# Optimization experiments

Hardware: AMD Instinct MI355X
Metric: run time of the kernel (lower is better)

## Reference

```python
import jax, jax.numpy as jnp
import numpy as np

B, S, D, H, FF = 1, 2048, 2048, 32, 8192
HD = D // H
SCALING = HD ** -0.5
WBITS, ABITS = 8, 8
NEG = jnp.finfo(jnp.float32).min


def ste_round(x):
    # straight-through estimator round
    return x + jax.lax.stop_gradient(jnp.round(x) - x)


def fake_quant(x, bits, axis):
    # min-max asymmetric fake quantization (OmniQuant-style dynamic quant)
    qmax = float(2 ** bits - 1)
    xmin = jnp.minimum(jnp.min(x, axis=axis, keepdims=True), 0.0)
    xmax = jnp.maximum(jnp.max(x, axis=axis, keepdims=True), 0.0)
    scale = jnp.maximum((xmax - xmin) / qmax, 1e-5)
    zp = jnp.round(-xmin / scale)
    q = jnp.clip(ste_round(x / scale) + zp, 0.0, qmax)
    return (q - zp) * scale


def qlinear(x, W, b):
    # QuantLinear: quantize activation per-token, weight per-output-channel
    xq = fake_quant(x, ABITS, -1)
    Wq = fake_quant(W, WBITS, 1)  # W: [out, in], per-row (output channel)
    return xq @ Wq.T + b


def layernorm(x, g, b):
    mu = jnp.mean(x, axis=-1, keepdims=True)
    var = jnp.var(x, axis=-1, keepdims=True)
    return (x - mu) * jax.lax.rsqrt(var + 1e-5) * g + b


def setup_inputs():
    key = jax.random.key(0)
    ks = jax.random.split(key, 16)
    w = lambda k, shape: (jax.random.normal(k, shape) * 0.02).astype(jnp.float32)
    hidden_states = jax.random.normal(ks[0], (B, S, D), dtype=jnp.float32)
    causal = jnp.tril(jnp.ones((S, S), dtype=bool))
    attention_mask = jnp.where(causal, 0.0, NEG)[None, None].astype(jnp.float32)
    attention_mask = jnp.broadcast_to(attention_mask, (B, 1, S, S))
    return {
        'hidden_states': hidden_states,
        'attention_mask': attention_mask,
        'Wq': w(ks[1], (D, D)), 'bq': jnp.zeros((D,), jnp.float32),
        'Wk': w(ks[2], (D, D)), 'bk': jnp.zeros((D,), jnp.float32),
        'Wv': w(ks[3], (D, D)), 'bv': jnp.zeros((D,), jnp.float32),
        'Wo': w(ks[4], (D, D)), 'bo': jnp.zeros((D,), jnp.float32),
        'ln1_g': jnp.ones((D,), jnp.float32), 'ln1_b': jnp.zeros((D,), jnp.float32),
        'W1': w(ks[5], (FF, D)), 'b1': jnp.zeros((FF,), jnp.float32),
        'W2': w(ks[6], (D, FF)), 'b2': jnp.zeros((D,), jnp.float32),
        'ln2_g': jnp.ones((D,), jnp.float32), 'ln2_b': jnp.zeros((D,), jnp.float32),
    }


def _split_heads(x):
    # [B,S,D] -> [B,H,S,HD]
    return x.reshape(B, S, H, HD).transpose(0, 2, 1, 3)


def _layer(hidden_states, attention_mask, Wq, bq, Wk, bk, Wv, bv, Wo, bo,
           ln1_g, ln1_b, W1, b1, W2, b2, ln2_g, ln2_b):
    # ---- self attention block (do_layer_norm_before=True) ----
    residual = hidden_states
    x = layernorm(hidden_states, ln1_g, ln1_b)

    q = qlinear(x, Wq, bq) * SCALING
    q = fake_quant(q, ABITS, -1)          # qkt_matmul.quant_x1
    k = qlinear(x, Wk, bk)
    k = fake_quant(k, ABITS, -1)          # qkt_matmul.quant_x2
    v = qlinear(x, Wv, bv)
    v = fake_quant(v, ABITS, -1)          # pv_matmul.quant_x2

    qh, kh, vh = _split_heads(q), _split_heads(k), _split_heads(v)
    scores = jnp.einsum('bhqd,bhkd->bhqk', qh, kh)  # [B,H,S,S]
    scores = scores + attention_mask
    scores = jnp.maximum(scores, NEG)
    probs = jax.nn.softmax(scores, axis=-1)
    probs = fake_quant(probs, ABITS, -1)  # pv_matmul.quant_x1
    ctx = jnp.einsum('bhqk,bhkd->bhqd', probs, vh)
    ctx = ctx.transpose(0, 2, 1, 3).reshape(B, S, D)
    attn_out = qlinear(ctx, Wo, bo)
    hidden_states = residual + attn_out

    # ---- FFN block ----
    residual = hidden_states
    x = layernorm(hidden_states, ln2_g, ln2_b)
    x = jax.nn.relu(qlinear(x, W1, b1))
    x = qlinear(x, W2, b2)
    return residual + x


def reference(hidden_states, attention_mask, Wq, bq, Wk, bk, Wv, bv, Wo, bo,
              ln1_g, ln1_b, W1, b1, W2, b2, ln2_g, ln2_b):
    return _layer(hidden_states, attention_mask, Wq, bq, Wk, bk, Wv, bv, Wo, bo,
                  ln1_g, ln1_b, W1, b1, W2, b2, ln2_g, ln2_b)
```

## Files before the change

kernel.cpp:

```cpp
#include <hip/hip_runtime.h>
#include <hip/hip_bf16.h>
#include <math.h>

#define S_LEN 2048
#define D_DIM 2048
#define H_NUM 32
#define HD_DIM 64
#define FF_DIM 8192
#define QMAX 255.0f
#define LOG2E 1.4426950408889634f

typedef __attribute__((ext_vector_type(4))) float f32x4;
typedef __attribute__((ext_vector_type(4))) int i32x4;
typedef __attribute__((ext_vector_type(8))) __bf16 bf16x8;
typedef unsigned short u16;
typedef signed char i8;

__device__ __forceinline__ u16 f32i_to_bf16(float v) {
  return (u16)(__float_as_uint(v) >> 16);
}
__device__ __forceinline__ u16 f32_to_bf16_rne(float v) {
  __bf16 b = (__bf16)v;
  return *(u16*)&b;
}
__device__ __forceinline__ float bf16_to_f32(u16 u) {
  return __uint_as_float((unsigned int)u << 16);
}
__device__ __forceinline__ int pack4_i8(float q0, float q1, float q2, float q3) {
  int c0 = (int)q0 - 128, c1 = (int)q1 - 128, c2 = (int)q2 - 128, c3 = (int)q3 - 128;
  return (c0 & 0xFF) | ((c1 & 0xFF) << 8) | ((c2 & 0xFF) << 16) | ((c3 & 0xFF) << 24);
}

__device__ __forceinline__ float wred_sum(float v) {
#pragma unroll
  for (int o = 1; o < 64; o <<= 1) v += __shfl_xor(v, o, 64);
  return v;
}
__device__ __forceinline__ float wred_min(float v) {
#pragma unroll
  for (int o = 1; o < 64; o <<= 1) v = fminf(v, __shfl_xor(v, o, 64));
  return v;
}
__device__ __forceinline__ float wred_max(float v) {
#pragma unroll
  for (int o = 1; o < 64; o <<= 1) v = fmaxf(v, __shfl_xor(v, o, 64));
  return v;
}

__device__ __forceinline__ void gload_lds16(const void* g, void* l) {
  __builtin_amdgcn_global_load_lds(
      (__attribute__((address_space(1))) void*)(g),
      (__attribute__((address_space(3))) void*)(l), 16, 0, 0);
}

__device__ __forceinline__ void xcd_swz(int& bx, int& by) {
  const int gx = gridDim.x;
  const int nwg = gx * gridDim.y;
  const int orig = blockIdx.x + gx * blockIdx.y;
  const int swz = (orig & 7) * (nwg >> 3) + (orig >> 3);
  bx = swz % gx;
  by = swz / gx;
}

__global__ __launch_bounds__(256) void ln_quant_i8(const float* __restrict__ x,
                                                   const float* __restrict__ g,
                                                   const float* __restrict__ bvec,
                                                   i8* __restrict__ out,
                                                   float* __restrict__ srow,
                                                   float* __restrict__ zrow,
                                                   float* __restrict__ S0row,
                                                   float* __restrict__ S1row) {
  __shared__ float red[8];
  const int row = blockIdx.x, tid = threadIdx.x;
  const float4* xr = (const float4*)(x + (size_t)row * D_DIM);
  const float4* g4 = (const float4*)g;
  const float4* b4 = (const float4*)bvec;

  float4 v0 = xr[tid], v1 = xr[tid + 256];
  float s = v0.x + v0.y + v0.z + v0.w + v1.x + v1.y + v1.z + v1.w;
  float ss = v0.x * v0.x + v0.y * v0.y + v0.z * v0.z + v0.w * v0.w +
             v1.x * v1.x + v1.y * v1.y + v1.z * v1.z + v1.w * v1.w;
  s = wred_sum(s); ss = wred_sum(ss);
  if ((tid & 63) == 0) { red[tid >> 6] = s; red[4 + (tid >> 6)] = ss; }
  __syncthreads();
  float mu = (red[0] + red[1] + red[2] + red[3]) / (float)D_DIM;
  float var = (red[4] + red[5] + red[6] + red[7]) / (float)D_DIM - mu * mu;
  float rstd = 1.0f / sqrtf(var + 1e-5f);
  __syncthreads();

  float mn = 0.f, mx = 0.f;
  float4 n0, n1;
  {
    float4 gg = g4[tid], bb = b4[tid];
    n0.x = (v0.x - mu) * rstd * gg.x + bb.x; n0.y = (v0.y - mu) * rstd * gg.y + bb.y;
    n0.z = (v0.z - mu) * rstd * gg.z + bb.z; n0.w = (v0.w - mu) * rstd * gg.w + bb.w;
    gg = g4[tid + 256]; bb = b4[tid + 256];
    n1.x = (v1.x - mu) * rstd * gg.x + bb.x; n1.y = (v1.y - mu) * rstd * gg.y + bb.y;
    n1.z = (v1.z - mu) * rstd * gg.z + bb.z; n1.w = (v1.w - mu) * rstd * gg.w + bb.w;
    mn = fminf(mn, fminf(fminf(n0.x, n0.y), fminf(n0.z, n0.w)));
    mn = fminf(mn, fminf(fminf(n1.x, n1.y), fminf(n1.z, n1.w)));
    mx = fmaxf(mx, fmaxf(fmaxf(n0.x, n0.y), fmaxf(n0.z, n0.w)));
    mx = fmaxf(mx, fmaxf(fmaxf(n1.x, n1.y), fmaxf(n1.z, n1.w)));
  }
  mn = wred_min(mn); mx = wred_max(mx);
  if ((tid & 63) == 0) { red[tid >> 6] = mn; red[4 + (tid >> 6)] = mx; }
  __syncthreads();
  mn = fminf(fminf(red[0], red[1]), fminf(red[2], red[3]));
  mx = fmaxf(fmaxf(red[4], red[5]), fmaxf(red[6], red[7]));
  float scale = fmaxf((mx - mn) / QMAX, 1e-5f);
  float zp = rintf(-mn / scale);
  if (tid == 0) { srow[row] = scale; zrow[row] = 128.0f - zp; }

  float q00 = fminf(fmaxf(rintf(n0.x / scale) + zp, 0.f), QMAX);
  float q01 = fminf(fmaxf(rintf(n0.y / scale) + zp, 0.f), QMAX);
  float q02 = fminf(fmaxf(rintf(n0.z / scale) + zp, 0.f), QMAX);
  float q03 = fminf(fmaxf(rintf(n0.w / scale) + zp, 0.f), QMAX);
  float q10 = fminf(fmaxf(rintf(n1.x / scale) + zp, 0.f), QMAX);
  float q11 = fminf(fmaxf(rintf(n1.y / scale) + zp, 0.f), QMAX);
  float q12 = fminf(fmaxf(rintf(n1.z / scale) + zp, 0.f), QMAX);
  float q13 = fminf(fmaxf(rintf(n1.w / scale) + zp, 0.f), QMAX);
  *(int*)&out[(size_t)row * D_DIM + tid * 4] = pack4_i8(q00, q01, q02, q03);
  *(int*)&out[(size_t)row * D_DIM + 1024 + tid * 4] = pack4_i8(q10, q11, q12, q13);
  float s0 = q00 + q01 + q02 + q03 - 512.f;
  float s1 = q10 + q11 + q12 + q13 - 512.f;
  __syncthreads();
  s0 = wred_sum(s0); s1 = wred_sum(s1);
  if ((tid & 63) == 0) { red[tid >> 6] = s0; red[4 + (tid >> 6)] = s1; }
  __syncthreads();
  if (tid == 0) {
    S0row[row] = red[0] + red[1] + red[2] + red[3];
    S1row[row] = red[4] + red[5] + red[6] + red[7];
  }
}

__global__ __launch_bounds__(256) void act_quant_i8(const float* __restrict__ x,
                                                    i8* __restrict__ out,
                                                    float* __restrict__ srow,
                                                    float* __restrict__ zrow,
                                                    float* __restrict__ S0row,
                                                    float* __restrict__ S1row) {
  __shared__ float red[8];
  const int row = blockIdx.x, tid = threadIdx.x;
  const float4* xr = (const float4*)(x + (size_t)row * D_DIM);
  float4 n0 = xr[tid], n1 = xr[tid + 256];
  float mn = 0.f, mx = 0.f;
  mn = fminf(mn, fminf(fminf(n0.x, n0.y), fminf(n0.z, n0.w)));
  mn = fminf(mn, fminf(fminf(n1.x, n1.y), fminf(n1.z, n1.w)));
  mx = fmaxf(mx, fmaxf(fmaxf(n0.x, n0.y), fmaxf(n0.z, n0.w)));
  mx = fmaxf(mx, fmaxf(fmaxf(n1.x, n1.y), fmaxf(n1.z, n1.w)));
  mn = wred_min(mn); mx = wred_max(mx);
  if ((tid & 63) == 0) { red[tid >> 6] = mn; red[4 + (tid >> 6)] = mx; }
  __syncthreads();
  mn = fminf(fminf(red[0], red[1]), fminf(red[2], red[3]));
  mx = fmaxf(fmaxf(red[4], red[5]), fmaxf(red[6], red[7]));
  float scale = fmaxf((mx - mn) / QMAX, 1e-5f);
  float zp = rintf(-mn / scale);
  if (tid == 0) { srow[row] = scale; zrow[row] = 128.0f - zp; }
  float q00 = fminf(fmaxf(rintf(n0.x / scale) + zp, 0.f), QMAX);
  float q01 = fminf(fmaxf(rintf(n0.y / scale) + zp, 0.f), QMAX);
  float q02 = fminf(fmaxf(rintf(n0.z / scale) + zp, 0.f), QMAX);
  float q03 = fminf(fmaxf(rintf(n0.w / scale) + zp, 0.f), QMAX);
  float q10 = fminf(fmaxf(rintf(n1.x / scale) + zp, 0.f), QMAX);
  float q11 = fminf(fmaxf(rintf(n1.y / scale) + zp, 0.f), QMAX);
  float q12 = fminf(fmaxf(rintf(n1.z / scale) + zp, 0.f), QMAX);
  float q13 = fminf(fmaxf(rintf(n1.w / scale) + zp, 0.f), QMAX);
  *(int*)&out[(size_t)row * D_DIM + tid * 4] = pack4_i8(q00, q01, q02, q03);
  *(int*)&out[(size_t)row * D_DIM + 1024 + tid * 4] = pack4_i8(q10, q11, q12, q13);
  float s0 = q00 + q01 + q02 + q03 - 512.f;
  float s1 = q10 + q11 + q12 + q13 - 512.f;
  __syncthreads();
  s0 = wred_sum(s0); s1 = wred_sum(s1);
  if ((tid & 63) == 0) { red[tid >> 6] = s0; red[4 + (tid >> 6)] = s1; }
  __syncthreads();
  if (tid == 0) {
    S0row[row] = red[0] + red[1] + red[2] + red[3];
    S1row[row] = red[4] + red[5] + red[6] + red[7];
  }
}

__device__ __forceinline__ void wquant_body(const float* __restrict__ wr0,
                                            i8* __restrict__ wo,
                                            float* __restrict__ sc,
                                            float* __restrict__ zc,
                                            float* __restrict__ S0c,
                                            float* __restrict__ S1c,
                                            int row, int K) {
  __shared__ float red[8];
  const int tid = threadIdx.x;
  const float4* wr = (const float4*)wr0;
  const int K4 = K >> 2, H4 = K4 >> 1;
  float mn = 0.f, mx = 0.f;
  for (int i = tid; i < K4; i += 256) {
    float4 v = wr[i];
    mn = fminf(mn, fminf(fminf(v.x, v.y), fminf(v.z, v.w)));
    mx = fmaxf(mx, fmaxf(fmaxf(v.x, v.y), fmaxf(v.z, v.w)));
  }
  mn = wred_min(mn); mx = wred_max(mx);
  if ((tid & 63) == 0) { red[tid >> 6] = mn; red[4 + (tid >> 6)] = mx; }
  __syncthreads();
  mn = fminf(fminf(red[0], red[1]), fminf(red[2], red[3]));
  mx = fmaxf(fmaxf(red[4], red[5]), fmaxf(red[6], red[7]));
  float scale = fmaxf((mx - mn) / QMAX, 1e-5f);
  float zp = rintf(-mn / scale);
  if (tid == 0) { sc[row] = scale; zc[row] = 128.0f - zp; }
  float s0 = 0.f, s1 = 0.f;
  for (int i = tid; i < K4; i += 256) {
    float4 v = wr[i];
    float q0 = fminf(fmaxf(rintf(v.x / scale) + zp, 0.f), QMAX);
    float q1 = fminf(fmaxf(rintf(v.y / scale) + zp, 0.f), QMAX);
    float q2 = fminf(fmaxf(rintf(v.z / scale) + zp, 0.f), QMAX);
    float q3 = fminf(fmaxf(rintf(v.w / scale) + zp, 0.f), QMAX);
    *(int*)&wo[i * 4] = pack4_i8(q0, q1, q2, q3);
    float gs = q0 + q1 + q2 + q3 - 512.f;
    if (i < H4) s0 += gs; else s1 += gs;
  }
  __syncthreads();
  s0 = wred_sum(s0); s1 = wred_sum(s1);
  if ((tid & 63) == 0) { red[tid >> 6] = s0; red[4 + (tid >> 6)] = s1; }
  __syncthreads();
  if (tid == 0) {
    S0c[row] = red[0] + red[1] + red[2] + red[3];
    S1c[row] = red[4] + red[5] + red[6] + red[7];
  }
}

__global__ __launch_bounds__(256) void wquant_i8(const float* __restrict__ W,
                                                 i8* __restrict__ Wi,
                                                 float* __restrict__ sc,
                                                 float* __restrict__ zc,
                                                 float* __restrict__ S0c,
                                                 float* __restrict__ S1c, int K) {
  const int row = blockIdx.x;
  wquant_body(W + (size_t)row * K, Wi + (size_t)row * K, sc, zc, S0c, S1c, row, K);
}

__global__ __launch_bounds__(256) void wquant4_i8(
    const float* __restrict__ W0, i8* __restrict__ O0, float* s0, float* z0, float* a0, float* b0,
    const float* __restrict__ W1, i8* __restrict__ O1, float* s1, float* z1, float* a1, float* b1,
    const float* __restrict__ W2, i8* __restrict__ O2, float* s2, float* z2, float* a2, float* b2,
    const float* __restrict__ W3, i8* __restrict__ O3, float* s3, float* z3, float* a3, float* b3) {
  const int which = blockIdx.x >> 11;
  const int row = blockIdx.x & (D_DIM - 1);
  const float* W = (which == 0) ? W0 : (which == 1) ? W1 : (which == 2) ? W2 : W3;
  i8* O = (which == 0) ? O0 : (which == 1) ? O1 : (which == 2) ? O2 : O3;
  float* sc = (which == 0) ? s0 : (which == 1) ? s1 : (which == 2) ? s2 : s3;
  float* zc = (which == 0) ? z0 : (which == 1) ? z1 : (which == 2) ? z2 : z3;
  float* Sa = (which == 0) ? a0 : (which == 1) ? a1 : (which == 2) ? a2 : a3;
  float* Sb = (which == 0) ? b0 : (which == 1) ? b1 : (which == 2) ? b2 : b3;
  wquant_body(W + (size_t)row * D_DIM, O + (size_t)row * D_DIM, sc, zc, Sa, Sb, row, D_DIM);
}

__global__ __launch_bounds__(256) void requant3(
    const u16* __restrict__ qv, const float* __restrict__ tqmn, const float* __restrict__ tqmx,
    u16* __restrict__ qo, float* __restrict__ sqv,
    const u16* __restrict__ kv, const float* __restrict__ tkmn, const float* __restrict__ tkmx,
    u16* __restrict__ ko, float* __restrict__ skv,
    const u16* __restrict__ vv, const float* __restrict__ tvmn, const float* __restrict__ tvmx,
    u16* __restrict__ vo) {
  __shared__ float red[8];
  const int wh = blockIdx.x >> 11;
  const int row = blockIdx.x & (S_LEN - 1);
  const int tid = threadIdx.x;
  const u16* vals = (wh == 0) ? qv : (wh == 1) ? kv : vv;
  const float* tmn = (wh == 0) ? tqmn : (wh == 1) ? tkmn : tvmn;
  const float* tmx = (wh == 0) ? tqmx : (wh == 1) ? tkmx : tvmx;
  u16* out = (wh == 0) ? qo : (wh == 1) ? ko : vo;
  float* srow = (wh == 0) ? sqv : (wh == 1) ? skv : nullptr;
  const int value_mode = (wh == 2) ? 1 : 0;

  float mn = 0.f, mx = 0.f;
  if (tid < 32) {
    mn = tmn[(size_t)row * 32 + tid];
    mx = tmx[(size_t)row * 32 + tid];
  }
  mn = wred_min(mn); mx = wred_max(mx);
  if ((tid & 63) == 0) { red[tid >> 6] = mn; red[4 + (tid >> 6)] = mx; }
  __syncthreads();
  mn = fminf(fminf(red[0], red[1]), fminf(red[2], red[3]));
  mx = fmaxf(fmaxf(red[4], red[5]), fmaxf(red[6], red[7]));
  mn = fminf(mn, 0.f); mx = fmaxf(mx, 0.f);
  float scale = fmaxf((mx - mn) / QMAX, 1e-5f);
  float zp = rintf(-mn / scale);
  if (srow && tid == 0) srow[row] = scale;
  const ushort4* vr = (const ushort4*)(vals + (size_t)row * D_DIM);
  ushort4* orow = (ushort4*)(out + (size_t)row * D_DIM);
  for (int i = tid; i < D_DIM / 4; i += 256) {
    ushort4 u = vr[i];
    float q0 = fminf(fmaxf(rintf(bf16_to_f32(u.x) / scale) + zp, 0.f), QMAX) - zp;
    float q1 = fminf(fmaxf(rintf(bf16_to_f32(u.y) / scale) + zp, 0.f), QMAX) - zp;
    float q2 = fminf(fmaxf(rintf(bf16_to_f32(u.z) / scale) + zp, 0.f), QMAX) - zp;
    float q3 = fminf(fmaxf(rintf(bf16_to_f32(u.w) / scale) + zp, 0.f), QMAX) - zp;
    ushort4 o;
    if (value_mode) {
      o.x = f32_to_bf16_rne(q0 * scale); o.y = f32_to_bf16_rne(q1 * scale);
      o.z = f32_to_bf16_rne(q2 * scale); o.w = f32_to_bf16_rne(q3 * scale);
    } else {
      o.x = f32i_to_bf16(q0); o.y = f32i_to_bf16(q1);
      o.z = f32i_to_bf16(q2); o.w = f32i_to_bf16(q3);
    }
    orow[i] = o;
  }
}

__global__ __launch_bounds__(256) void transpose_v(const u16* __restrict__ vfb,
                                                   u16* __restrict__ vtb) {
  __shared__ u16 Ts[64][66];
  const int j0 = blockIdx.x * 64;
  const int h = blockIdx.y;
  const int tid = threadIdx.x;
  for (int c = tid; c < 512; c += 256) {
    int r = c >> 3, ch = c & 7;
    *(float4*)&Ts[r][ch * 8] =
        *(const float4*)&vfb[(size_t)(j0 + r) * D_DIM + h * HD_DIM + ch * 8];
  }
  __syncthreads();
  for (int c = tid; c < 512; c += 256) {
    int d = c >> 3, ch = c & 7;
    u16 tmp[8];
#pragma unroll
    for (int e = 0; e < 8; ++e) tmp[e] = Ts[ch * 8 + e][d];
    *(float4*)&vtb[(size_t)(h * HD_DIM + d) * S_LEN + j0 + ch * 8] = *(float4*)tmp;
  }
}

__global__ __launch_bounds__(256) void requant_ff_i8(const u16* __restrict__ vals,
                                                     const float* __restrict__ tmx,
                                                     i8* __restrict__ out,
                                                     float* __restrict__ srow,
                                                     float* __restrict__ zrow,
                                                     float* __restrict__ S0row,
                                                     float* __restrict__ S1row) {
  __shared__ float red[8];
  const int row = blockIdx.x, tid = threadIdx.x;
  float mx = (tid < 128) ? tmx[(size_t)row * 128 + tid] : 0.f;
  mx = wred_max(mx);
  if ((tid & 63) == 0) red[tid >> 6] = mx;
  __syncthreads();
  mx = fmaxf(fmaxf(red[0], red[1]), fmaxf(red[2], red[3]));
  mx = fmaxf(mx, 0.f);
  float scale = fmaxf(mx / QMAX, 1e-5f);
  if (tid == 0) { srow[row] = scale; zrow[row] = 128.0f; }
  const ushort4* vr = (const ushort4*)(vals + (size_t)row * FF_DIM);
  const int N4 = FF_DIM >> 2;
  float s0 = 0.f, s1 = 0.f;
  for (int i = tid; i < N4; i += 256) {
    ushort4 u = vr[i];
    float q0 = fminf(fmaxf(rintf(bf16_to_f32(u.x) / scale), 0.f), QMAX);
    float q1 = fminf(fmaxf(rintf(bf16_to_f32(u.y) / scale), 0.f), QMAX);
    float q2 = fminf(fmaxf(rintf(bf16_to_f32(u.z) / scale), 0.f), QMAX);
    float q3 = fminf(fmaxf(rintf(bf16_to_f32(u.w) / scale), 0.f), QMAX);
    *(int*)&out[(size_t)row * FF_DIM + i * 4] = pack4_i8(q0, q1, q2, q3);
    float gs = q0 + q1 + q2 + q3 - 512.f;
    if (i < 1024) s0 += gs; else s1 += gs;
  }
  __syncthreads();
  s0 = wred_sum(s0); s1 = wred_sum(s1);
  if ((tid & 63) == 0) { red[tid >> 6] = s0; red[4 + (tid >> 6)] = s1; }
  __syncthreads();
  if (tid == 0) {
    S0row[row] = red[0] + red[1] + red[2] + red[3];
    S1row[row] = red[4] + red[5] + red[6] + red[7];
  }
}

__device__ __forceinline__ void gemm128_i8_db(
    const i8* __restrict__ A, const i8* __restrict__ B,
    int K, int bm, int bn, int k_begin, int k_end,
    i8* As, i8* Bs, i32x4 (&acc)[4][4]) {
  const int tid = threadIdx.x;
  const int wid = tid >> 6, lane = tid & 63;
  const int wr = wid >> 1, wc = wid & 1;
  const int lr = lane & 15, lk = lane >> 4;
  const int r0 = tid >> 2, c0 = (tid & 3) * 16;
  const int r1 = 64 + r0;
  const size_t ldsb0 = (size_t)(wid * 64) * 16;
  const size_t ldsb1 = (size_t)(256 + wid * 64) * 16;

  const i8* Ag0 = A + (size_t)(bm + r0) * K + c0;
  const i8* Ag1 = A + (size_t)(bm + r1) * K + c0;
  const i8* Bg0 = B + (size_t)(bn + r0) * K + c0;
  const i8* Bg1 = B + (size_t)(bn + r1) * K + c0;

  const int nt = (k_end - k_begin) >> 6;

#define STAGE_I8(t)                                   \
  {                                                   \
    const int _k = k_begin + (t) * 64;                \
    i8* _Ab = As + (size_t)((t) & 1) * 8192;          \
    i8* _Bb = Bs + (size_t)((t) & 1) * 8192;          \
    gload_lds16(Ag0 + _k, _Ab + ldsb0);               \
    gload_lds16(Ag1 + _k, _Ab + ldsb1);               \
    gload_lds16(Bg0 + _k, _Bb + ldsb0);               \
    gload_lds16(Bg1 + _k, _Bb + ldsb1);               \
  }

  STAGE_I8(0);
  __syncthreads();

  for (int t = 0; t < nt; ++t) {
    const i8* Ac = As + (size_t)(t & 1) * 8192;
    const i8* Bc = Bs + (size_t)(t & 1) * 8192;
    i32x4 af[4], bf[4];
// ... 173 lines not shown
#pragma unroll
      for (int r = 0; r < 4; ++r)
        dst[(size_t)(rbase + mi * 16 + r) * D_DIM + col] = (float)acc[mi][ni][r];
  }
}

__global__ __launch_bounds__(256) void splitk_reduce4(
    const float* __restrict__ part,
    const float* __restrict__ sxa, const float* __restrict__ zxa,
    const float* __restrict__ Sxa0, const float* __restrict__ Sxa1,
    const float* __restrict__ sw, const float* __restrict__ zw,
    const float* __restrict__ Sw0, const float* __restrict__ Sw1,
    float Kf, const float* __restrict__ bias, const float* __restrict__ res,
    float* __restrict__ out) {
  const size_t st4 = (size_t)S_LEN * D_DIM / 4;
  for (size_t i = (size_t)blockIdx.x * 256 + threadIdx.x; i < st4;
       i += (size_t)gridDim.x * 256) {
    const int row = (int)(i >> 9);
    const int c4 = (int)(i & 511);
    float4 s = ((const float4*)part)[i];
    float4 p1 = ((const float4*)part)[i + st4];
    float4 p2 = ((const float4*)part)[i + 2 * st4];
    float4 p3 = ((const float4*)part)[i + 3 * st4];
    s.x += p1.x + p2.x + p3.x; s.y += p1.y + p2.y + p3.y;
    s.z += p1.z + p2.z + p3.z; s.w += p1.w + p2.w + p3.w;
    const float sxr = sxa[row], zxr = zxa[row];
    const float Sxr = Sxa0[row] + Sxa1[row];
    float4 ws = ((const float4*)sw)[c4];
    float4 wz = ((const float4*)zw)[c4];
    float4 w0 = ((const float4*)Sw0)[c4];
    float4 w1 = ((const float4*)Sw1)[c4];
    float4 b4 = ((const float4*)bias)[c4];
    float4 o;
    o.x = sxr * ws.x * (s.x + zxr * (w0.x + w1.x) + wz.x * Sxr + Kf * zxr * wz.x) + b4.x;
    o.y = sxr * ws.y * (s.y + zxr * (w0.y + w1.y) + wz.y * Sxr + Kf * zxr * wz.y) + b4.y;
    o.z = sxr * ws.z * (s.z + zxr * (w0.z + w1.z) + wz.z * Sxr + Kf * zxr * wz.z) + b4.z;
    o.w = sxr * ws.w * (s.w + zxr * (w0.w + w1.w) + wz.w * Sxr + Kf * zxr * wz.w) + b4.w;
    if (res) {
      float4 r = ((const float4*)res)[i];
      o.x += r.x; o.y += r.y; o.z += r.z; o.w += r.w;
    }
    ((float4*)out)[i] = o;
  }
}

__global__ __launch_bounds__(256) void splitk_reduce_ln(
    const float* __restrict__ part,
    const float* __restrict__ sxa, const float* __restrict__ zxa,
    const float* __restrict__ Sxa0, const float* __restrict__ Sxa1,
    const float* __restrict__ sw, const float* __restrict__ zw,
    const float* __restrict__ Sw0, const float* __restrict__ Sw1,
    const float* __restrict__ bias, const float* __restrict__ res,
    float* __restrict__ h2out,
    const float* __restrict__ g, const float* __restrict__ bvec,
    i8* __restrict__ out, float* __restrict__ srow, float* __restrict__ zrow,
    float* __restrict__ S0row, float* __restrict__ S1row) {
  __shared__ float red[8];
  const int row = blockIdx.x, tid = threadIdx.x;
  const size_t st = (size_t)S_LEN * D_DIM;
  const float4* p0 = (const float4*)(part + (size_t)row * D_DIM);
  const float4* p1 = (const float4*)(part + st + (size_t)row * D_DIM);
  const float4* p2 = (const float4*)(part + 2 * st + (size_t)row * D_DIM);
  const float4* p3 = (const float4*)(part + 3 * st + (size_t)row * D_DIM);
  const float4* rr = (const float4*)(res + (size_t)row * D_DIM);
  const float4* b4 = (const float4*)bias;
  const float4* g4 = (const float4*)g;
  const float4* e4 = (const float4*)bvec;

  const float sxr = sxa[row], zxr = zxa[row];
  const float Sxr = Sxa0[row] + Sxa1[row];

  float4 v0, v1;
#pragma unroll
  for (int h = 0; h < 2; ++h) {
    const int idx = tid + h * 256;
    float4 a = p0[idx], q = p1[idx], u = p2[idx], w = p3[idx];
    float4 ws = ((const float4*)sw)[idx];
    float4 wz = ((const float4*)zw)[idx];
    float4 s0 = ((const float4*)Sw0)[idx];
    float4 s1 = ((const float4*)Sw1)[idx];
    float4 bb = b4[idx], rv = rr[idx];
    float4 o;
    o.x = sxr * ws.x * (a.x + q.x + u.x + w.x + zxr * (s0.x + s1.x) + wz.x * Sxr + 2048.0f * zxr * wz.x) + bb.x + rv.x;
    o.y = sxr * ws.y * (a.y + q.y + u.y + w.y + zxr * (s0.y + s1.y) + wz.y * Sxr + 2048.0f * zxr * wz.y) + bb.y + rv.y;
    o.z = sxr * ws.z * (a.z + q.z + u.z + w.z + zxr * (s0.z + s1.z) + wz.z * Sxr + 2048.0f * zxr * wz.z) + bb.z + rv.z;
    o.w = sxr * ws.w * (a.w + q.w + u.w + w.w + zxr * (s0.w + s1.w) + wz.w * Sxr + 2048.0f * zxr * wz.w) + bb.w + rv.w;
    if (h == 0) v0 = o; else v1 = o;
  }
  float* h2r = h2out + (size_t)row * D_DIM;
  *(float4*)&h2r[tid * 4] = v0;
  *(float4*)&h2r[1024 + tid * 4] = v1;

  float s = v0.x + v0.y + v0.z + v0.w + v1.x + v1.y + v1.z + v1.w;
  float ss = v0.x * v0.x + v0.y * v0.y + v0.z * v0.z + v0.w * v0.w +
             v1.x * v1.x + v1.y * v1.y + v1.z * v1.z + v1.w * v1.w;
  s = wred_sum(s); ss = wred_sum(ss);
  if ((tid & 63) == 0) { red[tid >> 6] = s; red[4 + (tid >> 6)] = ss; }
  __syncthreads();
  float mu = (red[0] + red[1] + red[2] + red[3]) / (float)D_DIM;
  float var = (red[4] + red[5] + red[6] + red[7]) / (float)D_DIM - mu * mu;
  float rstd = 1.0f / sqrtf(var + 1e-5f);
  __syncthreads();

  float mn = 0.f, mx = 0.f;
  float4 n0, n1;
  {
    float4 gg = g4[tid], bb = e4[tid];
    n0.x = (v0.x - mu) * rstd * gg.x + bb.x; n0.y = (v0.y - mu) * rstd * gg.y + bb.y;
    n0.z = (v0.z - mu) * rstd * gg.z + bb.z; n0.w = (v0.w - mu) * rstd * gg.w + bb.w;
    gg = g4[tid + 256]; bb = e4[tid + 256];
    n1.x = (v1.x - mu) * rstd * gg.x + bb.x; n1.y = (v1.y - mu) * rstd * gg.y + bb.y;
    n1.z = (v1.z - mu) * rstd * gg.z + bb.z; n1.w = (v1.w - mu) * rstd * gg.w + bb.w;
    mn = fminf(mn, fminf(fminf(n0.x, n0.y), fminf(n0.z, n0.w)));
    mn = fminf(mn, fminf(fminf(n1.x, n1.y), fminf(n1.z, n1.w)));
    mx = fmaxf(mx, fmaxf(fmaxf(n0.x, n0.y), fmaxf(n0.z, n0.w)));
    mx = fmaxf(mx, fmaxf(fmaxf(n1.x, n1.y), fmaxf(n1.z, n1.w)));
  }
  mn = wred_min(mn); mx = wred_max(mx);
  if ((tid & 63) == 0) { red[tid >> 6] = mn; red[4 + (tid >> 6)] = mx; }
  __syncthreads();
  mn = fminf(fminf(red[0], red[1]), fminf(red[2], red[3]));
  mx = fmaxf(fmaxf(red[4], red[5]), fmaxf(red[6], red[7]));
  float scale = fmaxf((mx - mn) / QMAX, 1e-5f);
  float zp = rintf(-mn / scale);
  if (tid == 0) { srow[row] = scale; zrow[row] = 128.0f - zp; }
  float q00 = fminf(fmaxf(rintf(n0.x / scale) + zp, 0.f), QMAX);
  float q01 = fminf(fmaxf(rintf(n0.y / scale) + zp, 0.f), QMAX);
  float q02 = fminf(fmaxf(rintf(n0.z / scale) + zp, 0.f), QMAX);
  float q03 = fminf(fmaxf(rintf(n0.w / scale) + zp, 0.f), QMAX);
  float q10 = fminf(fmaxf(rintf(n1.x / scale) + zp, 0.f), QMAX);
  float q11 = fminf(fmaxf(rintf(n1.y / scale) + zp, 0.f), QMAX);
  float q12 = fminf(fmaxf(rintf(n1.z / scale) + zp, 0.f), QMAX);
  float q13 = fminf(fmaxf(rintf(n1.w / scale) + zp, 0.f), QMAX);
  *(int*)&out[(size_t)row * D_DIM + tid * 4] = pack4_i8(q00, q01, q02, q03);
  *(int*)&out[(size_t)row * D_DIM + 1024 + tid * 4] = pack4_i8(q10, q11, q12, q13);
  float s0 = q00 + q01 + q02 + q03 - 512.f;
  float s1 = q10 + q11 + q12 + q13 - 512.f;
  __syncthreads();
  s0 = wred_sum(s0); s1 = wred_sum(s1);
  if ((tid & 63) == 0) { red[tid >> 6] = s0; red[4 + (tid >> 6)] = s1; }
  __syncthreads();
  if (tid == 0) {
    S0row[row] = red[0] + red[1] + red[2] + red[3];
    S1row[row] = red[4] + red[5] + red[6] + red[7];
  }
}

__global__ __launch_bounds__(256) void attn_ml(
    const u16* __restrict__ qi, const float* __restrict__ sq,
    const u16* __restrict__ ki, const float* __restrict__ sk,
    float* __restrict__ Mb, float* __restrict__ Lb) {
  __shared__ __align__(16) u16 Ks[64][72];
  const int bid = blockIdx.x;
  const int ti = (S_LEN / 64 - 1) - (bid >> 5);
  const int h = bid & (H_NUM - 1);
  const int i0 = ti * 64;
  const int tid = threadIdx.x;
  const int wid = tid >> 6, lane = tid & 63;
  const int lr = lane & 15, g = lane >> 4;
  const size_t hbase = (size_t)h * HD_DIM;

  const int r_a = tid >> 3, ch_a = tid & 7;
  const int r_b = 32 + r_a;

  const bf16x8 aq0 = *(const bf16x8*)&qi[(size_t)(i0 + wid * 16 + lr) * D_DIM + hbase + g * 8];
  const bf16x8 aq1 = *(const bf16x8*)&qi[(size_t)(i0 + wid * 16 + lr) * D_DIM + hbase + 32 + g * 8];
  float sq2[4];
#pragma unroll
  for (int r = 0; r < 4; ++r) sq2[r] = sq[i0 + wid * 16 + g * 4 + r] * LOG2E;

  const int ntiles = i0 / 64 + 1;
  float m_r[4] = {-1e30f, -1e30f, -1e30f, -1e30f};
  float l_r[4] = {0.f, 0.f, 0.f, 0.f};

  float4 ka0 = *(const float4*)&ki[(size_t)r_a * D_DIM + hbase + ch_a * 8];
  float4 ka1 = *(const float4*)&ki[(size_t)r_b * D_DIM + hbase + ch_a * 8];
  for (int t = 0; t < ntiles; ++t) {
    __syncthreads();
    *(float4*)&Ks[r_a][ch_a * 8] = ka0;
    *(float4*)&Ks[r_b][ch_a * 8] = ka1;
    __syncthreads();
    if (t + 1 < ntiles) {
      const int jn = (t + 1) * 64;
      ka0 = *(const float4*)&ki[(size_t)(jn + r_a) * D_DIM + hbase + ch_a * 8];
      ka1 = *(const float4*)&ki[(size_t)(jn + r_b) * D_DIM + hbase + ch_a * 8];
    }

    f32x4 accs[4] = {};
#pragma unroll
    for (int ni = 0; ni < 4; ++ni) {
      bf16x8 b0 = *(const bf16x8*)&Ks[ni * 16 + lr][g * 8];
      bf16x8 b1 = *(const bf16x8*)&Ks[ni * 16 + lr][32 + g * 8];
      accs[ni] = __builtin_amdgcn_mfma_f32_16x16x32_bf16(aq0, b0, accs[ni], 0, 0, 0);
      accs[ni] = __builtin_amdgcn_mfma_f32_16x16x32_bf16(aq1, b1, accs[ni], 0, 0, 0);
    }

    const int jt = t * 64;
    float tv[4][4];
#pragma unroll
    for (int ni = 0; ni < 4; ++ni) {
      const float skc = sk[jt + ni * 16 + lr];
#pragma unroll
      for (int r = 0; r < 4; ++r) tv[ni][r] = accs[ni][r] * sq2[r] * skc;
    }
    if (t == ntiles - 1) {
      const int jcol = jt + lr, irow = i0 + wid * 16 + g * 4;
#pragma unroll
      for (int ni = 0; ni < 4; ++ni)
#pragma unroll
        for (int r = 0; r < 4; ++r)
          if (jcol + ni * 16 > irow + r) tv[ni][r] = -1e30f;
    }
#pragma unroll
    for (int r = 0; r < 4; ++r) {
      float tmax = fmaxf(fmaxf(tv[0][r], tv[1][r]), fmaxf(tv[2][r], tv[3][r]));
      tmax = fmaxf(tmax, __shfl_xor(tmax, 1, 64));
      tmax = fmaxf(tmax, __shfl_xor(tmax, 2, 64));
      tmax = fmaxf(tmax, __shfl_xor(tmax, 4, 64));
      tmax = fmaxf(tmax, __shfl_xor(tmax, 8, 64));
      float mnew = fmaxf(m_r[r], tmax);
      float sum = exp2f(tv[0][r] - mnew) + exp2f(tv[1][r] - mnew) +
                  exp2f(tv[2][r] - mnew) + exp2f(tv[3][r] - mnew);
      sum += __shfl_xor(sum, 1, 64);
      sum += __shfl_xor(sum, 2, 64);
      sum += __shfl_xor(sum, 4, 64);
      sum += __shfl_xor(sum, 8, 64);
      l_r[r] = l_r[r] * exp2f(m_r[r] - mnew) + sum;
      m_r[r] = mnew;
    }
  }

  if (lr == 0) {
#pragma unroll
    for (int r = 0; r < 4; ++r) {
      const int row = i0 + wid * 16 + g * 4 + r;
      Mb[(size_t)h * S_LEN + row] = m_r[r];
      Lb[(size_t)h * S_LEN + row] = l_r[r];
    }
  }
}

__global__ __launch_bounds__(256) void attn_pv(
    const u16* __restrict__ qi, const float* __restrict__ sq,
    const u16* __restrict__ ki, const float* __restrict__ sk,
    const u16* __restrict__ vt,
    const float* __restrict__ Mb, const float* __restrict__ Lb,
    float* __restrict__ ctx) {
  __shared__ __align__(16) u16 Ks[64][72];
  __shared__ __align__(16) u16 Ps[64][72];
  __shared__ __align__(16) u16 Vt[64][72];
  const int bid = blockIdx.x;
  const int ti = (S_LEN / 64 - 1) - (bid >> 5);
  const int h = bid & (H_NUM - 1);
  const int i0 = ti * 64;
  const int tid = threadIdx.x;
  const int wid = tid >> 6, lane = tid & 63;
  const int lr = lane & 15, g = lane >> 4;
  const size_t hbase = (size_t)h * HD_DIM;
  const size_t vtbase = (size_t)h * HD_DIM * S_LEN;

  const int r_a = tid >> 3, ch_a = tid & 7;
  const int r_b = 32 + r_a;

  const bf16x8 aq0 = *(const bf16x8*)&qi[(size_t)(i0 + wid * 16 + lr) * D_DIM + hbase + g * 8];
  const bf16x8 aq1 = *(const bf16x8*)&qi[(size_t)(i0 + wid * 16 + lr) * D_DIM + hbase + 32 + g * 8];

  float sq2[4], b_r[4], qsc[4];
#pragma unroll
  for (int r = 0; r < 4; ++r) {
    const int row = i0 + wid * 16 + g * 4 + r;
    sq2[r] = sq[row] * LOG2E;
    float m_t = Mb[(size_t)h * S_LEN + row];
    float li = Lb[(size_t)h * S_LEN + row];
    float sc = fmaxf((1.0f / li) / QMAX, 1e-5f);
    qsc[r] = sc;
    b_r[r] = m_t - log2f(1.0f / (li * sc));
  }

  const int ntiles = i0 / 64 + 1;
  f32x4 acco[4] = {};
  float4 kb0 = *(const float4*)&ki[(size_t)r_a * D_DIM + hbase + ch_a * 8];
  float4 kb1 = *(const float4*)&ki[(size_t)r_b * D_DIM + hbase + ch_a * 8];
  float4 vb0 = *(const float4*)&vt[vtbase + (size_t)r_a * S_LEN + ch_a * 8];
  float4 vb1 = *(const float4*)&vt[vtbase + (size_t)r_b * S_LEN + ch_a * 8];
  for (int t = 0; t < ntiles; ++t) {
    __syncthreads();
    *(float4*)&Ks[r_a][ch_a * 8] = kb0;
    *(float4*)&Ks[r_b][ch_a * 8] = kb1;
    *(float4*)&Vt[r_a][ch_a * 8] = vb0;
    *(float4*)&Vt[r_b][ch_a * 8] = vb1;
    __syncthreads();
    if (t + 1 < ntiles) {
      const int jn = (t + 1) * 64;
      kb0 = *(const float4*)&ki[(size_t)(jn + r_a) * D_DIM + hbase + ch_a * 8];
      kb1 = *(const float4*)&ki[(size_t)(jn + r_b) * D_DIM + hbase + ch_a * 8];
      vb0 = *(const float4*)&vt[vtbase + (size_t)r_a * S_LEN + jn + ch_a * 8];
      vb1 = *(const float4*)&vt[vtbase + (size_t)r_b * S_LEN + jn + ch_a * 8];
    }

    f32x4 accs[4] = {};
#pragma unroll
    for (int ni = 0; ni < 4; ++ni) {
      bf16x8 b0 = *(const bf16x8*)&Ks[ni * 16 + lr][g * 8];
      bf16x8 b1 = *(const bf16x8*)&Ks[ni * 16 + lr][32 + g * 8];
      accs[ni] = __builtin_amdgcn_mfma_f32_16x16x32_bf16(aq0, b0, accs[ni], 0, 0, 0);
      accs[ni] = __builtin_amdgcn_mfma_f32_16x16x32_bf16(aq1, b1, accs[ni], 0, 0, 0);
    }

    const int jt = t * 64;
    const bool diag = (t == ntiles - 1);
    const int jcol = jt + lr, irow = i0 + wid * 16 + g * 4;
#pragma unroll
    for (int ni = 0; ni < 4; ++ni) {
      const float skc = sk[jt + ni * 16 + lr];
#pragma unroll
      for (int r = 0; r < 4; ++r) {
        float tvv = accs[ni][r] * sq2[r] * skc;
        if (diag && (jcol + ni * 16 > irow + r)) tvv = -1e30f;
        float q8 = fminf(rintf(exp2f(tvv - b_r[r])), QMAX);
        Ps[wid * 16 + g * 4 + r][ni * 16 + lr] = f32i_to_bf16(q8);
      }
    }

    bf16x8 ap0 = *(const bf16x8*)&Ps[wid * 16 + lr][g * 8];
    bf16x8 ap1 = *(const bf16x8*)&Ps[wid * 16 + lr][32 + g * 8];
#pragma unroll
    for (int ni = 0; ni < 4; ++ni) {
      bf16x8 b0 = *(const bf16x8*)&Vt[ni * 16 + lr][g * 8];
      bf16x8 b1 = *(const bf16x8*)&Vt[ni * 16 + lr][32 + g * 8];
      acco[ni] = __builtin_amdgcn_mfma_f32_16x16x32_bf16(ap0, b0, acco[ni], 0, 0, 0);
      acco[ni] = __builtin_amdgcn_mfma_f32_16x16x32_bf16(ap1, b1, acco[ni], 0, 0, 0);
    }
  }

#pragma unroll
  for (int ni = 0; ni < 4; ++ni)
#pragma unroll
    for (int r = 0; r < 4; ++r) {
      const int row = i0 + wid * 16 + g * 4 + r;
      ctx[(size_t)row * D_DIM + hbase + ni * 16 + lr] = acco[ni][r] * qsc[r];
    }
}

extern "C" void kernel_launch(void* const* d_in, const int* in_sizes, int n_in,
                              void* d_out, int out_size, void* d_ws, size_t ws_size,
                              hipStream_t stream) {
  (void)in_sizes; (void)n_in; (void)out_size;
  const float* hs  = (const float*)d_in[0];
  const float* Wq  = (const float*)d_in[2];
  const float* bq  = (const float*)d_in[3];
  const float* Wk  = (const float*)d_in[4];
  const float* bk  = (const float*)d_in[5];
  const float* Wv  = (const float*)d_in[6];
  const float* bv  = (const float*)d_in[7];
  const float* Wo  = (const float*)d_in[8];
  const float* bo  = (const float*)d_in[9];
  const float* g1  = (const float*)d_in[10];
  const float* be1 = (const float*)d_in[11];
  const float* W1  = (const float*)d_in[12];
  const float* bf1 = (const float*)d_in[13];
  const float* W2  = (const float*)d_in[14];
  const float* bf2 = (const float*)d_in[15];
  const float* g2  = (const float*)d_in[16];
  const float* be2 = (const float*)d_in[17];
  float* out = (float*)d_out;

  const size_t SD = (size_t)S_LEN * D_DIM;
  const size_t SF = (size_t)S_LEN * FF_DIM;
  const size_t HS = (size_t)H_NUM * S_LEN;

  char* p = (char*)d_ws;
  auto alloc = [&](size_t bytes) { char* r = p; p += (bytes + 255) & ~(size_t)255; return r; };

  float* h2   = (float*)alloc(SD * 4);
  float* sx   = (float*)alloc(S_LEN * 4);
  float* zx   = (float*)alloc(S_LEN * 4);
  float* Sx0  = (float*)alloc(S_LEN * 4);
  float* Sx1  = (float*)alloc(S_LEN * 4);
  float* sy   = (float*)alloc(S_LEN * 4);
  float* zy   = (float*)alloc(S_LEN * 4);
  float* Sy0  = (float*)alloc(S_LEN * 4);
  float* Sy1  = (float*)alloc(S_LEN * 4);
  float* sxf  = (float*)alloc(S_LEN * 4);
  float* zxf  = (float*)alloc(S_LEN * 4);
  float* Sf0  = (float*)alloc(S_LEN * 4);
  float* Sf1  = (float*)alloc(S_LEN * 4);
  float* sqv  = (float*)alloc(S_LEN * 4);
  float* skv  = (float*)alloc(S_LEN * 4);
  float* Mb   = (float*)alloc(HS * 4);
  float* Lbv  = (float*)alloc(HS * 4);
  float* swq = (float*)alloc(D_DIM * 4); float* zwq = (float*)alloc(D_DIM * 4);
  float* Sq0 = (float*)alloc(D_DIM * 4); float* Sq1 = (float*)alloc(D_DIM * 4);
  float* swk = (float*)alloc(D_DIM * 4); float* zwk = (float*)alloc(D_DIM * 4);
  float* Sk0 = (float*)alloc(D_DIM * 4); float* Sk1 = (float*)alloc(D_DIM * 4);
  float* swv = (float*)alloc(D_DIM * 4); float* zwv = (float*)alloc(D_DIM * 4);
  float* Sv0 = (float*)alloc(D_DIM * 4); float* Sv1 = (float*)alloc(D_DIM * 4);
  float* swo = (float*)alloc(D_DIM * 4); float* zwo = (float*)alloc(D_DIM * 4);
  float* So0 = (float*)alloc(D_DIM * 4); float* So1 = (float*)alloc(D_DIM * 4);
  float* sw1 = (float*)alloc(FF_DIM * 4); float* zw1 = (float*)alloc(FF_DIM * 4);
  float* S10 = (float*)alloc(FF_DIM * 4); float* S11 = (float*)alloc(FF_DIM * 4);
  float* sw2 = (float*)alloc(D_DIM * 4); float* zw2 = (float*)alloc(D_DIM * 4);
  float* S20 = (float*)alloc(D_DIM * 4); float* S21 = (float*)alloc(D_DIM * 4);
  float* tqmn = (float*)alloc(S_LEN * 32 * 4);
  float* tqmx = (float*)alloc(S_LEN * 32 * 4);
  float* tkmn = (float*)alloc(S_LEN * 32 * 4);
  float* tkmx = (float*)alloc(S_LEN * 32 * 4);
  float* tvmn = (float*)alloc(S_LEN * 32 * 4);
  float* tvmx = (float*)alloc(S_LEN * 32 * 4);
  float* tf1x = (float*)alloc(S_LEN * 128 * 4);
  i8* xi  = (i8*)alloc(SD);
  i8* wqi = (i8*)alloc(SD);
  i8* wki = (i8*)alloc(SD);
  i8* wvi = (i8*)alloc(SD);
  i8* woi = (i8*)alloc(SD);
  i8* w1i = (i8*)alloc(SF);
  i8* w2i = (i8*)alloc(SF);
  i8* f1i = (i8*)alloc(SF);
  char* arena = alloc(8 * SD * 2);
  u16* qv   = (u16*)arena;
  u16* kv   = qv + SD;
  u16* vv   = kv + SD;
  u16* qi8  = vv + SD;
  u16* ki8  = qi8 + SD;
  u16* vfb  = ki8 + SD;
  float* ctxb = (float*)(vfb + SD);
  u16* vtb  = qv;
  float* pwo = (float*)arena;
  u16* f1v = (u16*)arena;
  float* pw2 = (float*)arena;
  size_t need = (size_t)(p - (char*)d_ws);
  if (ws_size < need) return;

  dim3 blk(256);

  wquant4_i8<<<4 * D_DIM, blk, 0, stream>>>(
      Wq, wqi, swq, zwq, Sq0, Sq1,
      Wk, wki, swk, zwk, Sk0, Sk1,
      Wv, wvi, swv, zwv, Sv0, Sv1,
      Wo, woi, swo, zwo, So0, So1);
  wquant_i8<<<FF_DIM, blk, 0, stream>>>(W1, w1i, sw1, zw1, S10, S11, D_DIM);
  wquant_i8<<<D_DIM, blk, 0, stream>>>(W2, w2i, sw2, zw2, S20, S21, FF_DIM);

  ln_quant_i8<<<S_LEN, blk, 0, stream>>>(hs, g1, be1, xi, sx, zx, Sx0, Sx1);

  dim3 gqkv(3 * D_DIM / 128, S_LEN / 128);
  gemm_qkv_i8<<<gqkv, blk, 0, stream>>>(xi, sx, zx, Sx0, Sx1,
                                        wqi, swq, zwq, Sq0, Sq1, bq, qv, tqmn, tqmx,
                                        wki, swk, zwk, Sk0, Sk1, bk, kv, tkmn, tkmx,
                                        wvi, swv, zwv, Sv0, Sv1, bv, vv, tvmn, tvmx);

  requant3<<<3 * S_LEN, blk, 0, stream>>>(qv, tqmn, tqmx, qi8, sqv,
                                          kv, tkmn, tkmx, ki8, skv,
                                          vv, tvmn, tvmx, vfb);

  dim3 gtv(S_LEN / 64, H_NUM);
  transpose_v<<<gtv, blk, 0, stream>>>(vfb, vtb);

  const int ga = (S_LEN / 64) * H_NUM;
  attn_ml<<<ga, blk, 0, stream>>>(qi8, sqv, ki8, skv, Mb, Lbv);
  attn_pv<<<ga, blk, 0, stream>>>(qi8, sqv, ki8, skv, vtb, Mb, Lbv, ctxb);

  act_quant_i8<<<S_LEN, blk, 0, stream>>>(ctxb, xi, sx, zx, Sx0, Sx1);

  dim3 gwo(D_DIM / 128, S_LEN / 128, 4);
  gemm_splitk_i8<<<gwo, blk, 0, stream>>>(xi, woi, pwo, D_DIM, 4);
  splitk_reduce_ln<<<S_LEN, blk, 0, stream>>>(pwo, sx, zx, Sx0, Sx1,
                                              swo, zwo, So0, So1, bo, hs, h2,
                                              g2, be2, xi, sy, zy, Sy0, Sy1);

  dim3 gff(FF_DIM / 128, S_LEN / 128);
  gemm_w1_i8<<<gff, blk, 0, stream>>>(xi, sy, zy, Sy0, Sy1,
                                      w1i, sw1, zw1, S10, S11, bf1, f1v, tf1x);
  requant_ff_i8<<<S_LEN, blk, 0, stream>>>(f1v, tf1x, f1i, sxf, zxf, Sf0, Sf1);

  dim3 gw2(D_DIM / 128, S_LEN / 128, 4);
  gemm_splitk_i8<<<gw2, blk, 0, stream>>>(f1i, w2i, pw2, FF_DIM, 4);
  splitk_reduce4<<<2048, blk, 0, stream>>>(pw2, sxf, zxf, Sf0, Sf1,
                                           sw2, zw2, S20, S21, (float)FF_DIM,
                                           bf2, h2, out);
}
```

Baseline: 420.3 us.

## Register-cache weight rows in quant kernels, merge W1 launch, swizzle attention blocks

The weight quantization kernels now hold each row in registers after one global read, where before they read it twice (once for min/max, once to quantize). The W1 quantization is merged into the same launch as Q/K/V/O. Attention block indices are remapped so that blocks of the same head land on the same XCD for L2 reuse, and the GEMM XCD swizzle now walks the y dimension first. The cost is higher register use in the W2 kernel, which holds 8 float4 per thread.

```diff
diff --git a/kernel.cpp b/kernel.cpp
--- a/kernel.cpp
+++ b/kernel.cpp
@@ -54,12 +54,12 @@
 }
 
 __device__ __forceinline__ void xcd_swz(int& bx, int& by) {
-  const int gx = gridDim.x;
-  const int nwg = gx * gridDim.y;
-  const int orig = blockIdx.x + gx * blockIdx.y;
+  const int gy = gridDim.y;
+  const int nwg = gridDim.x * gy;
+  const int orig = blockIdx.y + gy * blockIdx.x;
   const int swz = (orig & 7) * (nwg >> 3) + (orig >> 3);
-  bx = swz % gx;
-  by = swz / gx;
+  by = swz % gy;
+  bx = swz / gy;
 }
 
 __global__ __launch_bounds__(256) void ln_quant_i8(const float* __restrict__ x,
@@ -178,22 +178,87 @@
   }
 }
 
-__device__ __forceinline__ void wquant_body(const float* __restrict__ wr0,
-                                            i8* __restrict__ wo,
-                                            float* __restrict__ sc,
-                                            float* __restrict__ zc,
-                                            float* __restrict__ S0c,
-                                            float* __restrict__ S1c,
-                                            int row, int K) {
+__device__ __forceinline__ void wquantD_body(const float* __restrict__ wr0,
+                                             i8* __restrict__ wo,
+                                             float* __restrict__ sc,
+                                             float* __restrict__ zc,
+                                             float* __restrict__ S0c,
+                                             float* __restrict__ S1c, int row) {
   __shared__ float red[8];
   const int tid = threadIdx.x;
   const float4* wr = (const float4*)wr0;
-  const int K4 = K >> 2, H4 = K4 >> 1;
+  float4 v0 = wr[tid], v1 = wr[tid + 256];
   float mn = 0.f, mx = 0.f;
-  for (int i = tid; i < K4; i += 256) {
-    float4 v = wr[i];
-    mn = fminf(mn, fminf(fminf(v.x, v.y), fminf(v.z, v.w)));
-    mx = fmaxf(mx, fmaxf(fmaxf(v.x, v.y), fmaxf(v.z, v.w)));
+  mn = fminf(mn, fminf(fminf(v0.x, v0.y), fminf(v0.z, v0.w)));
+  mn = fminf(mn, fminf(fminf(v1.x, v1.y), fminf(v1.z, v1.w)));
+  mx = fmaxf(mx, fmaxf(fmaxf(v0.x, v0.y), fmaxf(v0.z, v0.w)));
+  mx = fmaxf(mx, fmaxf(fmaxf(v1.x, v1.y), fmaxf(v1.z, v1.w)));
+  mn = wred_min(mn); mx = wred_max(mx);
+  if ((tid & 63) == 0) { red[tid >> 6] = mn; red[4 + (tid >> 6)] = mx; }
+  __syncthreads();
+  mn = fminf(fminf(red[0], red[1]), fminf(red[2], red[3]));
+  mx = fmaxf(fmaxf(red[4], red[5]), fmaxf(red[6], red[7]));
+  float scale = fmaxf((mx - mn) / QMAX, 1e-5f);
+  float zp = rintf(-mn / scale);
+  if (tid == 0) { sc[row] = scale; zc[row] = 128.0f - zp; }
+  float q00 = fminf(fmaxf(rintf(v0.x / scale) + zp, 0.f), QMAX);
+  float q01 = fminf(fmaxf(rintf(v0.y / scale) + zp, 0.f), QMAX);
+  float q02 = fminf(fmaxf(rintf(v0.z / scale) + zp, 0.f), QMAX);
+  float q03 = fminf(fmaxf(rintf(v0.w / scale) + zp, 0.f), QMAX);
+  float q10 = fminf(fmaxf(rintf(v1.x / scale) + zp, 0.f), QMAX);
+  float q11 = fminf(fmaxf(rintf(v1.y / scale) + zp, 0.f), QMAX);
+  float q12 = fminf(fmaxf(rintf(v1.z / scale) + zp, 0.f), QMAX);
+  float q13 = fminf(fmaxf(rintf(v1.w / scale) + zp, 0.f), QMAX);
+  *(int*)&wo[tid * 4] = pack4_i8(q00, q01, q02, q03);
+  *(int*)&wo[1024 + tid * 4] = pack4_i8(q10, q11, q12, q13);
+  float s0 = q00 + q01 + q02 + q03 - 512.f;
+  float s1 = q10 + q11 + q12 + q13 - 512.f;
+  __syncthreads();
+  s0 = wred_sum(s0); s1 = wred_sum(s1);
+  if ((tid & 63) == 0) { red[tid >> 6] = s0; red[4 + (tid >> 6)] = s1; }
+  __syncthreads();
+  if (tid == 0) {
+    S0c[row] = red[0] + red[1] + red[2] + red[3];
+    S1c[row] = red[4] + red[5] + red[6] + red[7];
+  }
+}
+
+__global__ __launch_bounds__(256) void wquantD_i8(
+    const float* __restrict__ Wq, i8* __restrict__ Oq, float* sq_, float* zq_, float* aq_, float* bq_,
+    const float* __restrict__ Wk, i8* __restrict__ Ok, float* sk_, float* zk_, float* ak_, float* bk_,
+    const float* __restrict__ Wv, i8* __restrict__ Ov, float* sv_, float* zv_, float* av_, float* bv_,
+    const float* __restrict__ Wo, i8* __restrict__ Oo, float* so_, float* zo_, float* ao_, float* bo_,
+    const float* __restrict__ W1, i8* __restrict__ O1, float* s1_, float* z1_, float* a1_, float* b1_) {
+  const int b = blockIdx.x;
+  int which, row;
+  if (b < 4 * D_DIM) { which = b >> 11; row = b & (D_DIM - 1); }
+  else { which = 4; row = b - 4 * D_DIM; }
+  const float* W = (which == 0) ? Wq : (which == 1) ? Wk : (which == 2) ? Wv : (which == 3) ? Wo : W1;
+  i8* O = (which == 0) ? Oq : (which == 1) ? Ok : (which == 2) ? Ov : (which == 3) ? Oo : O1;
+  float* sc = (which == 0) ? sq_ : (which == 1) ? sk_ : (which == 2) ? sv_ : (which == 3) ? so_ : s1_;
+  float* zc = (which == 0) ? zq_ : (which == 1) ? zk_ : (which == 2) ? zv_ : (which == 3) ? zo_ : z1_;
+  float* Sa = (which == 0) ? aq_ : (which == 1) ? ak_ : (which == 2) ? av_ : (which == 3) ? ao_ : a1_;
+  float* Sb = (which == 0) ? bq_ : (which == 1) ? bk_ : (which == 2) ? bv_ : (which == 3) ? bo_ : b1_;
+  wquantD_body(W + (size_t)row * D_DIM, O + (size_t)row * D_DIM, sc, zc, Sa, Sb, row);
+}
+
+__global__ __launch_bounds__(256) void wquantW2_i8(const float* __restrict__ W,
+                                                   i8* __restrict__ Wi,
+                                                   float* __restrict__ sc,
+                                                   float* __restrict__ zc,
+                                                   float* __restrict__ S0c,
+                                                   float* __restrict__ S1c) {
+  __shared__ float red[8];
+  const int row = blockIdx.x, tid = threadIdx.x;
+  const float4* wr = (const float4*)(W + (size_t)row * FF_DIM);
+  float4 v[8];
+#pragma unroll
+  for (int j = 0; j < 8; ++j) v[j] = wr[tid + 256 * j];
+  float mn = 0.f, mx = 0.f;
+#pragma unroll
+  for (int j = 0; j < 8; ++j) {
+    mn = fminf(mn, fminf(fminf(v[j].x, v[j].y), fminf(v[j].z, v[j].w)));
+    mx = fmaxf(mx, fmaxf(fmaxf(v[j].x, v[j].y), fmaxf(v[j].z, v[j].w)));
   }
   mn = wred_min(mn); mx = wred_max(mx);
   if ((tid & 63) == 0) { red[tid >> 6] = mn; red[4 + (tid >> 6)] = mx; }
@@ -204,15 +269,15 @@
   float zp = rintf(-mn / scale);
   if (tid == 0) { sc[row] = scale; zc[row] = 128.0f - zp; }
   float s0 = 0.f, s1 = 0.f;
-  for (int i = tid; i < K4; i += 256) {
-    float4 v = wr[i];
-    float q0 = fminf(fmaxf(rintf(v.x / scale) + zp, 0.f), QMAX);
-    float q1 = fminf(fmaxf(rintf(v.y / scale) + zp, 0.f), QMAX);
-    float q2 = fminf(fmaxf(rintf(v.z / scale) + zp, 0.f), QMAX);
-    float q3 = fminf(fmaxf(rintf(v.w / scale) + zp, 0.f), QMAX);
-    *(int*)&wo[i * 4] = pack4_i8(q0, q1, q2, q3);
+#pragma unroll
+  for (int j = 0; j < 8; ++j) {
+    float q0 = fminf(fmaxf(rintf(v[j].x / scale) + zp, 0.f), QMAX);
+    float q1 = fminf(fmaxf(rintf(v[j].y / scale) + zp, 0.f), QMAX);
+    float q2 = fminf(fmaxf(rintf(v[j].z / scale) + zp, 0.f), QMAX);
+    float q3 = fminf(fmaxf(rintf(v[j].w / scale) + zp, 0.f), QMAX);
+    *(int*)&Wi[(size_t)row * FF_DIM + (tid + 256 * j) * 4] = pack4_i8(q0, q1, q2, q3);
     float gs = q0 + q1 + q2 + q3 - 512.f;
-    if (i < H4) s0 += gs; else s1 += gs;
+    if (j < 4) s0 += gs; else s1 += gs;
   }
   __syncthreads();
   s0 = wred_sum(s0); s1 = wred_sum(s1);
@@ -222,32 +287,6 @@
     S0c[row] = red[0] + red[1] + red[2] + red[3];
     S1c[row] = red[4] + red[5] + red[6] + red[7];
   }
-}
-
-__global__ __launch_bounds__(256) void wquant_i8(const float* __restrict__ W,
-                                                 i8* __restrict__ Wi,
-                                                 float* __restrict__ sc,
-                                                 float* __restrict__ zc,
-                                                 float* __restrict__ S0c,
-                                                 float* __restrict__ S1c, int K) {
-  const int row = blockIdx.x;
-  wquant_body(W + (size_t)row * K, Wi + (size_t)row * K, sc, zc, S0c, S1c, row, K);
-}
-
-__global__ __launch_bounds__(256) void wquant4_i8(
-    const float* __restrict__ W0, i8* __restrict__ O0, float* s0, float* z0, float* a0, float* b0,
-    const float* __restrict__ W1, i8* __restrict__ O1, float* s1, float* z1, float* a1, float* b1,
-    const float* __restrict__ W2, i8* __restrict__ O2, float* s2, float* z2, float* a2, float* b2,
-    const float* __restrict__ W3, i8* __restrict__ O3, float* s3, float* z3, float* a3, float* b3) {
-  const int which = blockIdx.x >> 11;
-  const int row = blockIdx.x & (D_DIM - 1);
-  const float* W = (which == 0) ? W0 : (which == 1) ? W1 : (which == 2) ? W2 : W3;
-  i8* O = (which == 0) ? O0 : (which == 1) ? O1 : (which == 2) ? O2 : O3;
-  float* sc = (which == 0) ? s0 : (which == 1) ? s1 : (which == 2) ? s2 : s3;
-  float* zc = (which == 0) ? z0 : (which == 1) ? z1 : (which == 2) ? z2 : z3;
-  float* Sa = (which == 0) ? a0 : (which == 1) ? a1 : (which == 2) ? a2 : a3;
-  float* Sb = (which == 0) ? b0 : (which == 1) ? b1 : (which == 2) ? b2 : b3;
-  wquant_body(W + (size_t)row * D_DIM, O + (size_t)row * D_DIM, sc, zc, Sa, Sb, row, D_DIM);
 }
 
 __global__ __launch_bounds__(256) void requant3(
@@ -727,8 +766,9 @@
     float* __restrict__ Mb, float* __restrict__ Lb) {
   __shared__ __align__(16) u16 Ks[64][72];
   const int bid = blockIdx.x;
-  const int ti = (S_LEN / 64 - 1) - (bid >> 5);
-  const int h = bid & (H_NUM - 1);
+  const int swzb = (bid & 7) * ((S_LEN / 64 * H_NUM) >> 3) + (bid >> 3);
+  const int h = swzb >> 5;
+  const int ti = (S_LEN / 64 - 1) - (swzb & 31);
   const int i0 = ti * 64;
   const int tid = threadIdx.x;
   const int wid = tid >> 6, lane = tid & 63;
@@ -825,8 +865,9 @@
   __shared__ __align__(16) u16 Ps[64][72];
   __shared__ __align__(16) u16 Vt[64][72];
   const int bid = blockIdx.x;
-  const int ti = (S_LEN / 64 - 1) - (bid >> 5);
-  const int h = bid & (H_NUM - 1);
+  const int swzb = (bid & 7) * ((S_LEN / 64 * H_NUM) >> 3) + (bid >> 3);
+  const int h = swzb >> 5;
+  const int ti = (S_LEN / 64 - 1) - (swzb & 31);
   const int i0 = ti * 64;
   const int tid = threadIdx.x;
   const int wid = tid >> 6, lane = tid & 63;
@@ -1008,13 +1049,13 @@
 
   dim3 blk(256);
 
-  wquant4_i8<<<4 * D_DIM, blk, 0, stream>>>(
+  wquantD_i8<<<4 * D_DIM + FF_DIM, blk, 0, stream>>>(
       Wq, wqi, swq, zwq, Sq0, Sq1,
       Wk, wki, swk, zwk, Sk0, Sk1,
       Wv, wvi, swv, zwv, Sv0, Sv1,
-      Wo, woi, swo, zwo, So0, So1);
-  wquant_i8<<<FF_DIM, blk, 0, stream>>>(W1, w1i, sw1, zw1, S10, S11, D_DIM);
-  wquant_i8<<<D_DIM, blk, 0, stream>>>(W2, w2i, sw2, zw2, S20, S21, FF_DIM);
+      Wo, woi, swo, zwo, So0, So1,
+      W1, w1i, sw1, zw1, S10, S11);
+  wquantW2_i8<<<D_DIM, blk, 0, stream>>>(W2, w2i, sw2, zw2, S20, S21);
 
   ln_quant_i8<<<S_LEN, blk, 0, stream>>>(hs, g1, be1, xi, sx, zx, Sx0, Sx1);
 
```

New measurement: 468.2 us. 1.11x slower.
